# Kernel optimization log

Hardware: AMD Instinct MI355X
Metric: run time of the kernel (lower is better)

The kernel has to match this reference:

```python
import jax, jax.numpy as jnp
import numpy as np

# Irrep layout of node_vec: 128x0e | 64x1e (64*3) | 32x2e (32*5)
MUL0, MUL1, MUL2 = 128, 64, 32
A = 32  # node_attr scalar channels (32x0e)
N = 8192


def setup_inputs() -> dict:
    key = jax.random.key(0)
    ks = jax.random.split(key, 12)
    f32 = jnp.float32
    return {
        "node_vec": jax.random.normal(ks[0], (N, MUL0 + 3 * MUL1 + 5 * MUL2), f32),
        "node_embedding": jax.random.normal(ks[1], (N, A), f32),
        # fctp_1: TP(input, attr) -> gated irreps (scalars + gates + vectors)
        "W1s": jax.random.normal(ks[2], (MUL0, A, MUL0), f32),          # 0e x 0e -> 0e
        "b1s": jnp.zeros((MUL0,), f32),
        "W1g": jax.random.normal(ks[3], (MUL0, A, MUL1 + MUL2), f32),   # 0e x 0e -> gate 0e
        "b1g": jnp.zeros((MUL1 + MUL2,), f32),
        "W1v1": jax.random.normal(ks[4], (MUL1, A, MUL1), f32),         # 1e x 0e -> 1e
        "W1v2": jax.random.normal(ks[5], (MUL2, A, MUL2), f32),         # 2e x 0e -> 2e
        # fctp_2: TP(mlp_mid, attr) -> 32x0e (only scalar path allowed by CG rules)
        "W2": jax.random.normal(ks[6], (MUL0, A, A), f32),
        "b2": jnp.zeros((A,), f32),
        # output network: LinearRS(32->32) + SiLU + LinearRS(32->1)
        "W3": jax.random.normal(ks[7], (A, A), f32),
        "b3": jnp.zeros((A,), f32),
        "W4": jax.random.normal(ks[8], (A, 1), f32),
        "b4": jnp.zeros((1,), f32),
    }


def reference(node_vec, node_embedding, W1s, b1s, W1g, b1g, W1v1, W1v2, W2, b2, W3, b3, W4, b4):
    n = node_vec.shape[0]
    attr = node_embedding
    # split features by irrep degree
    s = node_vec[:, :MUL0]                                         # [n,128]   0e
    v1 = node_vec[:, MUL0:MUL0 + 3 * MUL1].reshape(n, MUL1, 3)     # [n,64,3]  1e
    v2 = node_vec[:, MUL0 + 3 * MUL1:].reshape(n, MUL2, 5)         # [n,32,5]  2e

    inv = lambda u: 1.0 / np.sqrt(u * A).astype(np.float32)

    # ---- fctp_1: fully-connected TP with scalar attr (l x 0e -> l per-path mixing) ----
    s_mid = jnp.einsum('nu,nv,uvw->nw', s, attr, W1s) * inv(MUL0) + b1s
    g = jnp.einsum('nu,nv,uvw->nw', s, attr, W1g) * inv(MUL0) + b1g
    v1_mid = jnp.einsum('num,nv,uvw->nwm', v1, attr, W1v1) * inv(MUL1)
    v2_mid = jnp.einsum('num,nv,uvw->nwm', v2, attr, W1v2) * inv(MUL2)

    # ---- SwishGate: SiLU on scalars, sigmoid gates on vectors ----
    s_act = jax.nn.silu(s_mid)
    gate = jax.nn.sigmoid(g)
    v1_g = v1_mid * gate[:, :MUL1, None]
    v2_g = v2_mid * gate[:, MUL1:, None]
    # NOTE: v1_g/v2_g have no allowed CG path into the 0e output of fctp_2 (l x 0 -> 0
    # only for l=0), so they do not contribute — exactly as in the original module.
    del v1_g, v2_g

    # ---- fctp_2: mlp_mid x attr -> 32x0e (scalar path only) ----
    h = jnp.einsum('nu,nv,uvw->nw', s_act, attr, W2) * inv(MUL0) + b2

    # ---- output network: LinearRS + SiLU + LinearRS ----
    h = jax.nn.silu(h @ (W3 / np.sqrt(A).astype(np.float32)) + b3)
    pred_energy = h @ (W4 / np.sqrt(A).astype(np.float32)) + b4     # [n,1]
    return pred_energy
```

## Files before the change

kernel.cpp:

```cpp
#include <hip/hip_runtime.h>

typedef _Float16 f16;
typedef f16 f16x8 __attribute__((ext_vector_type(8)));
typedef f16 f16x4 __attribute__((ext_vector_type(4)));
typedef f16 f16x2 __attribute__((ext_vector_type(2)));
typedef float f32x4 __attribute__((ext_vector_type(4)));

union F8 { uint4 u4; f16x8 v; f16x2 h[4]; f16 e[8]; };

__global__ __launch_bounds__(256) void prep_kernel(
    const float* __restrict__ W1s, const float* __restrict__ W2,
    f16* __restrict__ W1P, f16* __restrict__ W2P)
{
    __shared__ f16 T[32 * 36];
    const int b = blockIdx.x, t = threadIdx.x;

    const float* src; f16* dst; int u, w0, W;
    if (b < 512) { u = b >> 2; w0 = (b & 3) * 32; W = 128; src = W1s; dst = W1P; }
    else         { u = b - 512; w0 = 0;           W = 32;  src = W2;  dst = W2P; }
    {
        int v = t >> 3, wq = t & 7;
        float4 f = *(const float4*)(src + (size_t)(u * 32 + v) * W + w0 + wq * 4);
        T[v * 36 + wq * 4 + 0] = (f16)f.x;
        T[v * 36 + wq * 4 + 1] = (f16)f.y;
        T[v * 36 + wq * 4 + 2] = (f16)f.z;
        T[v * 36 + wq * 4 + 3] = (f16)f.w;
    }
    __syncthreads();
    {
        int w = t >> 3, vr = t & 7;
        f16x4 o = { T[(vr * 4 + 0) * 36 + w], T[(vr * 4 + 1) * 36 + w],
                    T[(vr * 4 + 2) * 36 + w], T[(vr * 4 + 3) * 36 + w] };
        *(f16x4*)(dst + (size_t)u * (W * 32) + (size_t)(w0 + w) * 32 + vr * 4) = o;
    }
}

__global__ __launch_bounds__(256, 2) void gemm1_kernel(
    const float* __restrict__ node_vec, const float* __restrict__ attr,
    const f16* __restrict__ W1P, const float* __restrict__ b1s,
    f16* __restrict__ s_act)
{
    __shared__ alignas(16) f16 s_lds[64 * 136];

    const int t  = threadIdx.x;
    const int n0 = blockIdx.x * 64;
    const int wv = t >> 6, l = t & 63, lr = l & 15, q = l >> 4;
    const int mtp = wv & 1, cs = wv >> 1;
    const int c0 = blockIdx.y * 64 + cs * 32;
    const int r0 = 32 * mtp;

    #pragma unroll
    for (int i = 0; i < 8; ++i) {
        int idx = t + 256 * i;
        int r = idx >> 5, c4 = idx & 31;
        float4 f = *(const float4*)(node_vec + (size_t)(n0 + r) * 480 + c4 * 4);
        f16x4 o = { (f16)f.x, (f16)f.y, (f16)f.z, (f16)f.w };
        *(f16x4*)(s_lds + r * 136 + c4 * 4) = o;
    }

    F8 af0, af1;
    #pragma unroll
    for (int kk = 0; kk < 4; ++kk) {
        float2 fa = *(const float2*)(attr + (size_t)(n0 + r0 + lr) * 32 + q * 8 + kk * 2);
        float2 fb = *(const float2*)(attr + (size_t)(n0 + r0 + 16 + lr) * 32 + q * 8 + kk * 2);
        af0.h[kk] = f16x2{ (f16)fa.x, (f16)fa.y };
        af1.h[kk] = f16x2{ (f16)fb.x, (f16)fb.y };
    }

    const f16* Bp = W1P + ((size_t)(c0 + lr)) * 32 + q * 8;
    f16x8 B0[8], B1[8];
    #pragma unroll
    for (int j = 0; j < 8; ++j) {
        B0[j] = *(const f16x8*)(Bp + (size_t)j * 4096);
        B1[j] = *(const f16x8*)(Bp + (size_t)j * 4096 + 512);
    }

    __syncthreads();

    f32x4 acc00 = {0,0,0,0}, acc01 = {0,0,0,0};
    f32x4 acc10 = {0,0,0,0}, acc11 = {0,0,0,0};

    F8 s8[2][2];
    s8[0][0].v = *(const f16x8*)(s_lds + (r0 + lr) * 136);
    s8[0][1].v = *(const f16x8*)(s_lds + (r0 + 16 + lr) * 136);

    #pragma unroll
    for (int uo = 0; uo < 16; ++uo) {
        const int cur = uo & 1, nxt = cur ^ 1;
        const int uon = (uo + 1 < 16) ? uo + 1 : 15;
        s8[nxt][0].v = *(const f16x8*)(s_lds + (r0 + lr) * 136 + uon * 8);
        s8[nxt][1].v = *(const f16x8*)(s_lds + (r0 + 16 + lr) * 136 + uon * 8);
        #pragma unroll
        for (int j = 0; j < 8; ++j) {
            const int u = uo * 8 + j;
            f16x8 bf0 = B0[j], bf1 = B1[j];
            const int un = (u + 8 < 128) ? (u + 8) : u;
            B0[j] = *(const f16x8*)(Bp + (size_t)un * 4096);
            B1[j] = *(const f16x8*)(Bp + (size_t)un * 4096 + 512);
            f16 sv0 = s8[cur][0].e[j];
            f16 sv1 = s8[cur][1].e[j];
            f16x2 sb0 = { sv0, sv0 }, sb1 = { sv1, sv1 };
            F8 a0, a1;
            #pragma unroll
            for (int kk = 0; kk < 4; ++kk) {
                a0.h[kk] = sb0 * af0.h[kk];
                a1.h[kk] = sb1 * af1.h[kk];
            }
            acc00 = __builtin_amdgcn_mfma_f32_16x16x32_f16(a0.v, bf0, acc00, 0, 0, 0);
            acc01 = __builtin_amdgcn_mfma_f32_16x16x32_f16(a0.v, bf1, acc01, 0, 0, 0);
            acc10 = __builtin_amdgcn_mfma_f32_16x16x32_f16(a1.v, bf0, acc10, 0, 0, 0);
            acc11 = __builtin_amdgcn_mfma_f32_16x16x32_f16(a1.v, bf1, acc11, 0, 0, 0);
        }
    }

    const float bv0 = b1s[c0 + lr];
    const float bv1 = b1s[c0 + 16 + lr];
    #pragma unroll
    for (int reg = 0; reg < 4; ++reg) {
        int ra = n0 + r0 + q * 4 + reg;
        int rb = n0 + r0 + 16 + q * 4 + reg;
        float v00 = acc00[reg] * 0.015625f + bv0;
        float v01 = acc01[reg] * 0.015625f + bv1;
        float v10 = acc10[reg] * 0.015625f + bv0;
        float v11 = acc11[reg] * 0.015625f + bv1;
        s_act[(size_t)ra * 128 + c0 + lr]      = (f16)(v00 / (1.f + __expf(-v00)));
        s_act[(size_t)ra * 128 + c0 + 16 + lr] = (f16)(v01 / (1.f + __expf(-v01)));
        s_act[(size_t)rb * 128 + c0 + lr]      = (f16)(v10 / (1.f + __expf(-v10)));
        s_act[(size_t)rb * 128 + c0 + 16 + lr] = (f16)(v11 / (1.f + __expf(-v11)));
    }
}

__global__ __launch_bounds__(256, 2) void gemm2_head_kernel(
    const f16* __restrict__ s_act, const float* __restrict__ attr,
    const f16* __restrict__ W2P, const float* __restrict__ b2,
    const float* __restrict__ W3, const float* __restrict__ b3,
    const float* __restrict__ W4, const float* __restrict__ b4,
    float* __restrict__ out)
{
    __shared__ alignas(16) f16 s_lds[32 * 136];
    __shared__ alignas(16) float red[4][32 * 36];
    __shared__ alignas(16) float W3_lds[32 * 36];
    __shared__ alignas(16) float h_lds[32 * 36];

    const int t  = threadIdx.x;
    const int n0 = blockIdx.x * 32;
    const int wv = t >> 6, l = t & 63, lr = l & 15, q = l >> 4;
    const int u0 = wv * 32;

    const f16* B2p = W2P + ((size_t)u0 * 32 + lr) * 32 + q * 8;
    f16x8 B0[8], B1[8];
    #pragma unroll
    for (int j = 0; j < 8; ++j) {
        B0[j] = *(const f16x8*)(B2p + (size_t)j * 1024);
        B1[j] = *(const f16x8*)(B2p + (size_t)j * 1024 + 512);
    }

    F8 af0, af1;
    #pragma unroll
    for (int kk = 0; kk < 4; ++kk) {
        float2 fa = *(const float2*)(attr + (size_t)(n0 + lr) * 32 + q * 8 + kk * 2);
        float2 fb = *(const float2*)(attr + (size_t)(n0 + 16 + lr) * 32 + q * 8 + kk * 2);
        af0.h[kk] = f16x2{ (f16)fa.x, (f16)fa.y };
        af1.h[kk] = f16x2{ (f16)fb.x, (f16)fb.y };
    }

    #pragma unroll
    for (int i = 0; i < 2; ++i) {
        int ch = t + 256 * i;
        int r = ch >> 4, c8 = ch & 15;
        *(uint4*)(s_lds + r * 136 + c8 * 8) =
            *(const uint4*)(s_act + (size_t)(n0 + r) * 128 + c8 * 8);
    }
    { int i = t >> 3, jj = (t & 7) * 4;
      *(f32x4*)(W3_lds + i * 36 + jj) = *(const f32x4*)(W3 + i * 32 + jj); }
    __syncthreads();

    f32x4 acc00 = {0,0,0,0}, acc01 = {0,0,0,0};
    f32x4 acc10 = {0,0,0,0}, acc11 = {0,0,0,0};

    F8 s8[2][2];
    s8[0][0].v = *(const f16x8*)(s_lds + lr * 136 + u0);
    s8[0][1].v = *(const f16x8*)(s_lds + (16 + lr) * 136 + u0);

    #pragma unroll
    for (int uo = 0; uo < 4; ++uo) {
        const int cur = uo & 1, nxt = cur ^ 1;
        const int uon = (uo + 1 < 4) ? uo + 1 : 3;
        s8[nxt][0].v = *(const f16x8*)(s_lds + lr * 136 + u0 + uon * 8);
        s8[nxt][1].v = *(const f16x8*)(s_lds + (16 + lr) * 136 + u0 + uon * 8);
        #pragma unroll
        for (int j = 0; j < 8; ++j) {
            const int k = uo * 8 + j;
            f16x8 bf0 = B0[j], bf1 = B1[j];
            const int kn = (k + 8 < 32) ? (k + 8) : k;
            B0[j] = *(const f16x8*)(B2p + (size_t)kn * 1024);
            B1[j] = *(const f16x8*)(B2p + (size_t)kn * 1024 + 512);
            f16 sv0 = s8[cur][0].e[j];
            f16 sv1 = s8[cur][1].e[j];
            f16x2 sb0 = { sv0, sv0 }, sb1 = { sv1, sv1 };
            F8 a0, a1;
            #pragma unroll
            for (int kk = 0; kk < 4; ++kk) {
                a0.h[kk] = sb0 * af0.h[kk];
                a1.h[kk] = sb1 * af1.h[kk];
            }
            acc00 = __builtin_amdgcn_mfma_f32_16x16x32_f16(a0.v, bf0, acc00, 0, 0, 0);
            acc01 = __builtin_amdgcn_mfma_f32_16x16x32_f16(a0.v, bf1, acc01, 0, 0, 0);
            acc10 = __builtin_amdgcn_mfma_f32_16x16x32_f16(a1.v, bf0, acc10, 0, 0, 0);
            acc11 = __builtin_amdgcn_mfma_f32_16x16x32_f16(a1.v, bf1, acc11, 0, 0, 0);
        }
    }

    #pragma unroll
    for (int reg = 0; reg < 4; ++reg) {
        red[wv][(q * 4 + reg) * 36 + lr]           = acc00[reg];
        red[wv][(q * 4 + reg) * 36 + 16 + lr]      = acc01[reg];
        red[wv][(16 + q * 4 + reg) * 36 + lr]      = acc10[reg];
        red[wv][(16 + q * 4 + reg) * 36 + 16 + lr] = acc11[reg];
    }
    __syncthreads();

    {
        int row = t >> 3, c4 = (t & 7) * 4;
        f32x4 s = *(const f32x4*)(&red[0][row * 36 + c4]);
        s = s + *(const f32x4*)(&red[1][row * 36 + c4]);
        s = s + *(const f32x4*)(&red[2][row * 36 + c4]);
        s = s + *(const f32x4*)(&red[3][row * 36 + c4]);
        #pragma unroll
        for (int e = 0; e < 4; ++e)
            h_lds[row * 36 + c4 + e] = s[e] * 0.015625f + b2[c4 + e];
    }
    __syncthreads();

    {
        int node = t >> 3, j4 = (t & 7) * 4;
        float a0 = 0.f, a1 = 0.f, a2 = 0.f, a3 = 0.f;
        #pragma unroll
        for (int i = 0; i < 32; ++i) {
            float hv = h_lds[node * 36 + i];
            a0 += hv * W3_lds[i * 36 + j4 + 0];
            a1 += hv * W3_lds[i * 36 + j4 + 1];
            a2 += hv * W3_lds[i * 36 + j4 + 2];
            a3 += hv * W3_lds[i * 36 + j4 + 3];
        }
        const float inv = 0.17677669529663687f;
        float p = 0.f;
        float aa[4] = { a0, a1, a2, a3 };
        #pragma unroll
        for (int e = 0; e < 4; ++e) {
            float tv = aa[e] * inv + b3[j4 + e];
            float g  = tv / (1.f + __expf(-tv));
            p += g * W4[j4 + e] * inv;
        }
        p += __shfl_xor(p, 1);
        p += __shfl_xor(p, 2);
        p += __shfl_xor(p, 4);
        if ((t & 7) == 0) out[n0 + node] = p + b4[0];
    }
}

extern "C" void kernel_launch(void* const* d_in, const int* in_sizes, int n_in,
                              void* d_out, int out_size, void* d_ws, size_t ws_size,
                              hipStream_t stream)
{
    const float* node_vec = (const float*)d_in[0];
    const float* attr     = (const float*)d_in[1];
    const float* W1s      = (const float*)d_in[2];
    const float* b1s      = (const float*)d_in[3];
    const float* W2       = (const float*)d_in[8];
    const float* b2       = (const float*)d_in[9];
    const float* W3       = (const float*)d_in[10];
    const float* b3       = (const float*)d_in[11];
    const float* W4       = (const float*)d_in[12];
    const float* b4       = (const float*)d_in[13];
    float* out = (float*)d_out;

    char* ws = (char*)d_ws;
    f16* W1P   = (f16*)(ws);
    f16* W2P   = (f16*)(ws + (1u << 20));
    f16* s_act = (f16*)(ws + (1280u << 10));

    prep_kernel<<<640, 256, 0, stream>>>(W1s, W2, W1P, W2P);
    gemm1_kernel<<<dim3(128, 2), 256, 0, stream>>>(node_vec, attr, W1P, b1s, s_act);
    gemm2_head_kernel<<<256, 256, 0, stream>>>(s_act, attr, W2P, b2,
                                               W3, b3, W4, b4, out);
}
```

Before: 119.8 us.

## Fuse gemm1 and gemm2/head into one kernel keeping activations in LDS

Merges the first tensor-product GEMM with the second GEMM and output head into a single 512-thread kernel. Each block handles 64 nodes and all 128 output channels. The SiLU activations stay in shared memory instead of making a round trip through a global workspace, which also removes one kernel launch. In exchange the grid shrinks to 128 blocks, fewer than the number of CUs, and LDS use per block grows considerably.

```diff
diff --git a/kernel.cpp b/kernel.cpp
--- a/kernel.cpp
+++ b/kernel.cpp
@@ -35,27 +35,47 @@
     }
 }
 
-__global__ __launch_bounds__(256, 2) void gemm1_kernel(
+__global__ __launch_bounds__(512, 2) void fused_kernel(
     const float* __restrict__ node_vec, const float* __restrict__ attr,
-    const f16* __restrict__ W1P, const float* __restrict__ b1s,
-    f16* __restrict__ s_act)
+    const f16* __restrict__ W1P, const f16* __restrict__ W2P,
+    const float* __restrict__ b1s, const float* __restrict__ b2,
+    const float* __restrict__ W3, const float* __restrict__ b3,
+    const float* __restrict__ W4, const float* __restrict__ b4,
+    float* __restrict__ out)
 {
     __shared__ alignas(16) f16 s_lds[64 * 136];
+    __shared__ alignas(16) f16 sact_lds[64 * 136];
+    __shared__ alignas(16) float red[4][64 * 36];
+    __shared__ alignas(16) float W3_lds[32 * 36];
+    __shared__ alignas(16) float h_lds[64 * 36];
 
     const int t  = threadIdx.x;
     const int n0 = blockIdx.x * 64;
     const int wv = t >> 6, l = t & 63, lr = l & 15, q = l >> 4;
-    const int mtp = wv & 1, cs = wv >> 1;
-    const int c0 = blockIdx.y * 64 + cs * 32;
-    const int r0 = 32 * mtp;
-
-    #pragma unroll
-    for (int i = 0; i < 8; ++i) {
-        int idx = t + 256 * i;
+    const int wm = wv & 1;
+    const int cs = wv >> 1;
+    const int r0 = 32 * wm;
+    const int c0 = 32 * cs;
+
+    const f16* Bp = W1P + ((size_t)(c0 + lr)) * 32 + q * 8;
+    f16x8 B0[8], B1[8];
+    #pragma unroll
+    for (int j = 0; j < 8; ++j) {
+        B0[j] = *(const f16x8*)(Bp + (size_t)j * 4096);
+        B1[j] = *(const f16x8*)(Bp + (size_t)j * 4096 + 512);
+    }
+
+    #pragma unroll
+    for (int i = 0; i < 4; ++i) {
+        int idx = t + 512 * i;
         int r = idx >> 5, c4 = idx & 31;
         float4 f = *(const float4*)(node_vec + (size_t)(n0 + r) * 480 + c4 * 4);
         f16x4 o = { (f16)f.x, (f16)f.y, (f16)f.z, (f16)f.w };
         *(f16x4*)(s_lds + r * 136 + c4 * 4) = o;
+    }
+    if (t < 256) {
+        int i = t >> 3, jj = (t & 7) * 4;
+        *(f32x4*)(W3_lds + i * 36 + jj) = *(const f32x4*)(W3 + i * 32 + jj);
     }
 
     F8 af0, af1;
@@ -65,14 +85,6 @@
         float2 fb = *(const float2*)(attr + (size_t)(n0 + r0 + 16 + lr) * 32 + q * 8 + kk * 2);
         af0.h[kk] = f16x2{ (f16)fa.x, (f16)fa.y };
         af1.h[kk] = f16x2{ (f16)fb.x, (f16)fb.y };
-    }
-
-    const f16* Bp = W1P + ((size_t)(c0 + lr)) * 32 + q * 8;
-    f16x8 B0[8], B1[8];
-    #pragma unroll
-    for (int j = 0; j < 8; ++j) {
-        B0[j] = *(const f16x8*)(Bp + (size_t)j * 4096);
-        B1[j] = *(const f16x8*)(Bp + (size_t)j * 4096 + 512);
     }
 
     __syncthreads();
@@ -113,90 +125,58 @@
         }
     }
 
-    const float bv0 = b1s[c0 + lr];
-    const float bv1 = b1s[c0 + 16 + lr];
-    #pragma unroll
-    for (int reg = 0; reg < 4; ++reg) {
-        int ra = n0 + r0 + q * 4 + reg;
-        int rb = n0 + r0 + 16 + q * 4 + reg;
-        float v00 = acc00[reg] * 0.015625f + bv0;
-        float v01 = acc01[reg] * 0.015625f + bv1;
-        float v10 = acc10[reg] * 0.015625f + bv0;
-        float v11 = acc11[reg] * 0.015625f + bv1;
-        s_act[(size_t)ra * 128 + c0 + lr]      = (f16)(v00 / (1.f + __expf(-v00)));
-        s_act[(size_t)ra * 128 + c0 + 16 + lr] = (f16)(v01 / (1.f + __expf(-v01)));
-        s_act[(size_t)rb * 128 + c0 + lr]      = (f16)(v10 / (1.f + __expf(-v10)));
-        s_act[(size_t)rb * 128 + c0 + 16 + lr] = (f16)(v11 / (1.f + __expf(-v11)));
-    }
-}
-
-__global__ __launch_bounds__(256, 2) void gemm2_head_kernel(
-    const f16* __restrict__ s_act, const float* __restrict__ attr,
-    const f16* __restrict__ W2P, const float* __restrict__ b2,
-    const float* __restrict__ W3, const float* __restrict__ b3,
-    const float* __restrict__ W4, const float* __restrict__ b4,
-    float* __restrict__ out)
-{
-    __shared__ alignas(16) f16 s_lds[32 * 136];
-    __shared__ alignas(16) float red[4][32 * 36];
-    __shared__ alignas(16) float W3_lds[32 * 36];
-    __shared__ alignas(16) float h_lds[32 * 36];
-
-    const int t  = threadIdx.x;
-    const int n0 = blockIdx.x * 32;
-    const int wv = t >> 6, l = t & 63, lr = l & 15, q = l >> 4;
-    const int u0 = wv * 32;
-
-    const f16* B2p = W2P + ((size_t)u0 * 32 + lr) * 32 + q * 8;
-    f16x8 B0[8], B1[8];
+    {
+        const float bv0 = b1s[c0 + lr];
+        const float bv1 = b1s[c0 + 16 + lr];
+        #pragma unroll
+        for (int reg = 0; reg < 4; ++reg) {
+            int ra = r0 + q * 4 + reg;
+            int rb = r0 + 16 + q * 4 + reg;
+            float v00 = acc00[reg] * 0.015625f + bv0;
+            float v01 = acc01[reg] * 0.015625f + bv1;
+            float v10 = acc10[reg] * 0.015625f + bv0;
+            float v11 = acc11[reg] * 0.015625f + bv1;
+            sact_lds[ra * 136 + c0 + lr]      = (f16)(v00 / (1.f + __expf(-v00)));
+            sact_lds[ra * 136 + c0 + 16 + lr] = (f16)(v01 / (1.f + __expf(-v01)));
+            sact_lds[rb * 136 + c0 + lr]      = (f16)(v10 / (1.f + __expf(-v10)));
+            sact_lds[rb * 136 + c0 + 16 + lr] = (f16)(v11 / (1.f + __expf(-v11)));
+        }
+    }
+    __syncthreads();
+
+    const int ku = wv >> 1;
+    const int u0 = 32 * ku;
+
+    const f16* B2p = W2P + (size_t)u0 * 1024 + (size_t)lr * 32 + q * 8;
+    f16x8 C0[8], C1[8];
     #pragma unroll
     for (int j = 0; j < 8; ++j) {
-        B0[j] = *(const f16x8*)(B2p + (size_t)j * 1024);
-        B1[j] = *(const f16x8*)(B2p + (size_t)j * 1024 + 512);
-    }
-
-    F8 af0, af1;
-    #pragma unroll
-    for (int kk = 0; kk < 4; ++kk) {
-        float2 fa = *(const float2*)(attr + (size_t)(n0 + lr) * 32 + q * 8 + kk * 2);
-        float2 fb = *(const float2*)(attr + (size_t)(n0 + 16 + lr) * 32 + q * 8 + kk * 2);
-        af0.h[kk] = f16x2{ (f16)fa.x, (f16)fa.y };
-        af1.h[kk] = f16x2{ (f16)fb.x, (f16)fb.y };
-    }
-
-    #pragma unroll
-    for (int i = 0; i < 2; ++i) {
-        int ch = t + 256 * i;
-        int r = ch >> 4, c8 = ch & 15;
-        *(uint4*)(s_lds + r * 136 + c8 * 8) =
-            *(const uint4*)(s_act + (size_t)(n0 + r) * 128 + c8 * 8);
-    }
-    { int i = t >> 3, jj = (t & 7) * 4;
-      *(f32x4*)(W3_lds + i * 36 + jj) = *(const f32x4*)(W3 + i * 32 + jj); }
-    __syncthreads();
-
-    f32x4 acc00 = {0,0,0,0}, acc01 = {0,0,0,0};
-    f32x4 acc10 = {0,0,0,0}, acc11 = {0,0,0,0};
-
-    F8 s8[2][2];
-    s8[0][0].v = *(const f16x8*)(s_lds + lr * 136 + u0);
-    s8[0][1].v = *(const f16x8*)(s_lds + (16 + lr) * 136 + u0);
+        C0[j] = *(const f16x8*)(B2p + (size_t)j * 1024);
+        C1[j] = *(const f16x8*)(B2p + (size_t)j * 1024 + 512);
+    }
+
+    f32x4 d00 = {0,0,0,0}, d01 = {0,0,0,0};
+    f32x4 d10 = {0,0,0,0}, d11 = {0,0,0,0};
+
+    F8 t8[2][2];
+    t8[0][0].v = *(const f16x8*)(sact_lds + (r0 + lr) * 136 + u0);
+    t8[0][1].v = *(const f16x8*)(sact_lds + (r0 + 16 + lr) * 136 + u0);
 
     #pragma unroll
     for (int uo = 0; uo < 4; ++uo) {
         const int cur = uo & 1, nxt = cur ^ 1;
         const int uon = (uo + 1 < 4) ? uo + 1 : 3;
-        s8[nxt][0].v = *(const f16x8*)(s_lds + lr * 136 + u0 + uon * 8);
-        s8[nxt][1].v = *(const f16x8*)(s_lds + (16 + lr) * 136 + u0 + uon * 8);
+        t8[nxt][0].v = *(const f16x8*)(sact_lds + (r0 + lr) * 136 + u0 + uon * 8);
+        t8[nxt][1].v = *(const f16x8*)(sact_lds + (r0 + 16 + lr) * 136 + u0 + uon * 8);
         #pragma unroll
         for (int j = 0; j < 8; ++j) {
             const int k = uo * 8 + j;
-            f16x8 bf0 = B0[j], bf1 = B1[j];
+            f16x8 cf0 = C0[j], cf1 = C1[j];
             const int kn = (k + 8 < 32) ? (k + 8) : k;
-            B0[j] = *(const f16x8*)(B2p + (size_t)kn * 1024);
-            B1[j] = *(const f16x8*)(B2p + (size_t)kn * 1024 + 512);
-            f16 sv0 = s8[cur][0].e[j];
-            f16 sv1 = s8[cur][1].e[j];
+            C0[j] = *(const f16x8*)(B2p + (size_t)kn * 1024);
+            C1[j] = *(const f16x8*)(B2p + (size_t)kn * 1024 + 512);
+            f16 sv0 = t8[cur][0].e[j];
+            f16 sv1 = t8[cur][1].e[j];
             f16x2 sb0 = { sv0, sv0 }, sb1 = { sv1, sv1 };
             F8 a0, a1;
             #pragma unroll
@@ -204,19 +184,19 @@
                 a0.h[kk] = sb0 * af0.h[kk];
                 a1.h[kk] = sb1 * af1.h[kk];
             }
-            acc00 = __builtin_amdgcn_mfma_f32_16x16x32_f16(a0.v, bf0, acc00, 0, 0, 0);
-            acc01 = __builtin_amdgcn_mfma_f32_16x16x32_f16(a0.v, bf1, acc01, 0, 0, 0);
-            acc10 = __builtin_amdgcn_mfma_f32_16x16x32_f16(a1.v, bf0, acc10, 0, 0, 0);
-            acc11 = __builtin_amdgcn_mfma_f32_16x16x32_f16(a1.v, bf1, acc11, 0, 0, 0);
+            d00 = __builtin_amdgcn_mfma_f32_16x16x32_f16(a0.v, cf0, d00, 0, 0, 0);
+            d01 = __builtin_amdgcn_mfma_f32_16x16x32_f16(a0.v, cf1, d01, 0, 0, 0);
+            d10 = __builtin_amdgcn_mfma_f32_16x16x32_f16(a1.v, cf0, d10, 0, 0, 0);
+            d11 = __builtin_amdgcn_mfma_f32_16x16x32_f16(a1.v, cf1, d11, 0, 0, 0);
         }
     }
 
     #pragma unroll
     for (int reg = 0; reg < 4; ++reg) {
-        red[wv][(q * 4 + reg) * 36 + lr]           = acc00[reg];
-        red[wv][(q * 4 + reg) * 36 + 16 + lr]      = acc01[reg];
-        red[wv][(16 + q * 4 + reg) * 36 + lr]      = acc10[reg];
-        red[wv][(16 + q * 4 + reg) * 36 + 16 + lr] = acc11[reg];
+        red[ku][(r0 + q * 4 + reg) * 36 + lr]           = d00[reg];
+        red[ku][(r0 + q * 4 + reg) * 36 + 16 + lr]      = d01[reg];
+        red[ku][(r0 + 16 + q * 4 + reg) * 36 + lr]      = d10[reg];
+        red[ku][(r0 + 16 + q * 4 + reg) * 36 + 16 + lr] = d11[reg];
     }
     __syncthreads();
 
@@ -276,12 +256,10 @@
     float* out = (float*)d_out;
 
     char* ws = (char*)d_ws;
-    f16* W1P   = (f16*)(ws);
-    f16* W2P   = (f16*)(ws + (1u << 20));
-    f16* s_act = (f16*)(ws + (1280u << 10));
+    f16* W1P = (f16*)(ws);
+    f16* W2P = (f16*)(ws + (1u << 20));
 
     prep_kernel<<<640, 256, 0, stream>>>(W1s, W2, W1P, W2P);
-    gemm1_kernel<<<dim3(128, 2), 256, 0, stream>>>(node_vec, attr, W1P, b1s, s_act);
-    gemm2_head_kernel<<<256, 256, 0, stream>>>(s_act, attr, W2P, b2,
-                                               W3, b3, W4, b4, out);
+    fused_kernel<<<128, 512, 0, stream>>>(node_vec, attr, W1P, W2P,
+                                          b1s, b2, W3, b3, W4, b4, out);
 }
```

Result: slower. 128.6 us (+7.4%).
